# Optimization experiments

Measured on AMD Instinct MI355X. Metric: run time of the kernel, lower is better.

The kernel has to match this reference:

```python
import jax, jax.numpy as jnp
import numpy as np

B, N, C, K, D, H = 4, 16384, 256, 16, 4, 512
EPS = 1e-5


def setup_inputs() -> dict:
    key = jax.random.key(0)
    ks = jax.random.split(key, 16)
    s = 0.05  # weight scale
    inp = {
        "x": jax.random.normal(ks[0], (B, N, C), jnp.float32),
        "knn": jax.random.randint(ks[1], (B, N, K), 0, N, jnp.int32),
        "lfp_w": jax.random.normal(ks[2], (D, C, C), jnp.float32) * s,
        "lfp_bn_w": jax.random.uniform(ks[3], (D, C), jnp.float32),
        "lfp_bn_b": jax.random.normal(ks[4], (D, C), jnp.float32) * s,
        "mlp0_w1": jax.random.normal(ks[5], (C, H), jnp.float32) * s,
        "mlp0_b1": jax.random.normal(ks[6], (H,), jnp.float32) * s,
        "mlp0_w2": jax.random.normal(ks[7], (H, C), jnp.float32) * s,
        "mlp0_bn_w": jax.random.uniform(ks[8], (C,), jnp.float32),
        "mlp0_bn_b": jax.random.normal(ks[9], (C,), jnp.float32) * s,
        "mlps_w1": jax.random.normal(ks[10], (D // 2, C, H), jnp.float32) * s,
        "mlps_b1": jax.random.normal(ks[11], (D // 2, H), jnp.float32) * s,
        "mlps_w2": jax.random.normal(ks[12], (D // 2, H, C), jnp.float32) * s,
        "mlps_bn_w": jax.random.uniform(ks[13], (D // 2, C), jnp.float32),
        "mlps_bn_b": jax.random.normal(ks[14], (D // 2, C), jnp.float32) * s,
    }
    return inp


def _bn(y, w, b):
    # BatchNorm1d over flattened (B*N) rows, biased variance, train-mode stats
    m = y.mean(axis=(0, 1))
    v = ((y - m) ** 2).mean(axis=(0, 1))
    return (y - m) * jax.lax.rsqrt(v + EPS) * w + b


def _mlp(y, w1, b1, w2, bw, bb):
    h = jax.nn.gelu(jnp.einsum("bnc,ch->bnh", y, w1) + b1, approximate=False)
    return _bn(jnp.einsum("bnh,hc->bnc", h, w2), bw, bb)


def _lfp(y, knn, w, bw, bb):
    p = jnp.einsum("bnc,cd->bnd", y, w)               # linear proj, no bias
    nb = jax.vmap(lambda pb, kb: pb[kb])(p, knn)      # [B,N,K,C] neighbor gather
    return _bn(nb.max(axis=2) - p, bw, bb)            # max over knn minus self


def reference(x, knn, lfp_w, lfp_bn_w, lfp_bn_b,
              mlp0_w1, mlp0_b1, mlp0_w2, mlp0_bn_w, mlp0_bn_b,
              mlps_w1, mlps_b1, mlps_w2, mlps_bn_w, mlps_bn_b):
    # Block.forward (eval: drop_path = identity)
    x = x + _mlp(x, mlp0_w1, mlp0_b1, mlp0_w2, mlp0_bn_w, mlp0_bn_b)
    depth = lfp_w.shape[0]
    for i in range(depth):
        x = x + _lfp(x, knn, lfp_w[i], lfp_bn_w[i], lfp_bn_b[i])
        if i % 2 == 1:
            j = i // 2
            x = x + _mlp(x, mlps_w1[j], mlps_b1[j], mlps_w2[j],
                         mlps_bn_w[j], mlps_bn_b[j])
    return x
```

## Files before the change

### kernel.cpp

```cpp
#include <hip/hip_runtime.h>
#include <hip/hip_bf16.h>

#define M_TOTAL 65536
#define NPTS    16384
#define CDIM    256
#define KNN     16
#define HDIM    512
#define CSTR    136

typedef __bf16 bf16x8 __attribute__((ext_vector_type(8)));
typedef float  f32x4  __attribute__((ext_vector_type(4)));

__device__ inline float b2f(unsigned u) {
    union { unsigned v; float f; } x; x.v = u << 16; return x.f;
}
__device__ inline unsigned short f2b(float f) {
    union { float f; unsigned u; } x; x.f = f;
    unsigned r = x.u + 0x7fffu + ((x.u >> 16) & 1u);
    return (unsigned short)(r >> 16);
}
__device__ inline void gload_lds16(const void* g, void* l) {
    __builtin_amdgcn_global_load_lds(
        (const __attribute__((address_space(1))) unsigned*)g,
        (__attribute__((address_space(3))) unsigned*)l, 16, 0, 0);
}
__device__ inline float gelu_tanh(float u) {
    const float t = u * (0.7978845608f + 0.0356774081f * u * u);
    const float e = __expf(2.f * t);
    const float th = 1.f - 2.f * __builtin_amdgcn_rcpf(e + 1.f);
    return 0.5f * u * (1.f + th);
}
__device__ inline void fmax8(uint4 v, float* mx) {
    mx[0] = fmaxf(mx[0], b2f(v.x & 0xffffu)); mx[1] = fmaxf(mx[1], b2f(v.x >> 16));
    mx[2] = fmaxf(mx[2], b2f(v.y & 0xffffu)); mx[3] = fmaxf(mx[3], b2f(v.y >> 16));
    mx[4] = fmaxf(mx[4], b2f(v.z & 0xffffu)); mx[5] = fmaxf(mx[5], b2f(v.z >> 16));
    mx[6] = fmaxf(mx[6], b2f(v.w & 0xffffu)); mx[7] = fmaxf(mx[7], b2f(v.w >> 16));
}

template<int MODE>
__global__ __launch_bounds__(256) void gemm_nt(
    const short* __restrict__ A, const short* __restrict__ BT,
    short* __restrict__ outB,
    const float* __restrict__ bias, float2* __restrict__ partials,
    int N, int K)
{
    __shared__ short a_lds[128 * 32];
    __shared__ short b_lds[128 * 32];
    __shared__ short c_lds[128 * CSTR];
    __shared__ float s_sum[128], s_sq[128];

    const int tid = threadIdx.x;
    const int nx = gridDim.x, nwg = nx * gridDim.y;
    const int bid = blockIdx.y * nx + blockIdx.x;
    const int lid = (bid & 7) * (nwg >> 3) + (bid >> 3);
    const int m0 = (lid / nx) * 128, n0 = (lid % nx) * 128;

    const int w = tid >> 6, l = tid & 63;
    const int wm = w >> 1, wn = w & 1;

    if (MODE == 2 && tid < 128) { s_sum[tid] = 0.f; s_sq[tid] = 0.f; }

    f32x4 acc[4][4] = {};

    const int lrow = l & 15, lk = (l >> 4) * 8;
    const int q0 = 2 * w, q1 = 2 * w + 1;
    const int gr = l >> 2, gc = (l & 3) * 8;
    const size_t arow0 = (size_t)(m0 + q0 * 16 + gr) * K + gc;
    const size_t arow1 = (size_t)(m0 + q1 * 16 + gr) * K + gc;
    const size_t brow0 = (size_t)(n0 + q0 * 16 + gr) * K + gc;
    const size_t brow1 = (size_t)(n0 + q1 * 16 + gr) * K + gc;

    const int nkt = K >> 5;
    for (int kt = 0; kt < nkt; ++kt) {
        const int k0 = kt << 5;
        if (kt) __syncthreads();
        gload_lds16(A  + arow0 + k0, a_lds + q0 * 512);
        gload_lds16(A  + arow1 + k0, a_lds + q1 * 512);
        gload_lds16(BT + brow0 + k0, b_lds + q0 * 512);
        gload_lds16(BT + brow1 + k0, b_lds + q1 * 512);
        __syncthreads();

        bf16x8 af[4], bfr[4];
#pragma unroll
        for (int i = 0; i < 4; ++i)
            af[i] = *(const bf16x8*)(a_lds + (wm * 64 + i * 16 + lrow) * 32 + lk);
#pragma unroll
        for (int j = 0; j < 4; ++j)
            bfr[j] = *(const bf16x8*)(b_lds + (wn * 64 + j * 16 + lrow) * 32 + lk);
#pragma unroll
        for (int i = 0; i < 4; ++i)
#pragma unroll
            for (int j = 0; j < 4; ++j)
                acc[i][j] = __builtin_amdgcn_mfma_f32_16x16x32_bf16(
                    af[i], bfr[j], acc[i][j], 0, 0, 0);
    }

    const int lq = l >> 4;
#pragma unroll
    for (int j = 0; j < 4; ++j) {
        const int cl  = wn * 64 + j * 16 + lrow;
        const float bsv = (MODE == 1) ? bias[n0 + cl] : 0.f;
        float psum = 0.f, psq = 0.f;
#pragma unroll
        for (int i = 0; i < 4; ++i) {
#pragma unroll
            for (int r = 0; r < 4; ++r) {
                const int row = wm * 64 + i * 16 + lq * 4 + r;
                float v = acc[i][j][r];
                if (MODE == 1) v = gelu_tanh(v + bsv);
                c_lds[row * CSTR + cl] = (short)f2b(v);
                if (MODE == 2) { psum += v; psq += v * v; }
            }
        }
        if (MODE == 2) {
            atomicAdd(&s_sum[cl], psum);
            atomicAdd(&s_sq[cl], psq);
        }
    }
    __syncthreads();
#pragma unroll
    for (int it = 0; it < 8; ++it) {
        const int idx = it * 256 + tid;
        const int row = idx >> 4, ch = idx & 15;
        const uint4 vv = *(const uint4*)&c_lds[row * CSTR + ch * 8];
        *(uint4*)&outB[(size_t)(m0 + row) * N + n0 + ch * 8] = vv;
    }
    if (MODE == 2 && tid < 128)
        partials[(size_t)(m0 >> 7) * N + n0 + tid] =
            make_float2(s_sum[tid], s_sq[tid]);
}

__global__ __launch_bounds__(256) void gather_max(
    const short* __restrict__ p, const int* __restrict__ knn,
    short* __restrict__ yout, float2* __restrict__ partials)
{
    __shared__ float s_sum[256], s_sq[256];
    const int tid = threadIdx.x, w = tid >> 6, l = tid & 63;
    s_sum[tid] = 0.f; s_sq[tid] = 0.f;
    __syncthreads();

    const int xcd = blockIdx.x & 7, hi = blockIdx.x >> 3;
    const int gblk = (xcd >> 1) * 512 + (hi << 1) + (xcd & 1);

    const int sub = l >> 5;
    const int cl8 = (l & 31) * 8;

    float sa[8] = {}, qa[8] = {};
    for (int it = 0; it < 4; ++it) {
        const size_t g = (size_t)gblk * 32 + w * 8 + it * 2 + sub;
        const int b = (int)(g >> 14);
        const int4* kp4 = (const int4*)(knn) + g * 4;
        const int4 k0 = kp4[0], k1 = kp4[1], k2 = kp4[2], k3 = kp4[3];
        int idxs[16];
        idxs[0]=k0.x; idxs[1]=k0.y; idxs[2]=k0.z; idxs[3]=k0.w;
        idxs[4]=k1.x; idxs[5]=k1.y; idxs[6]=k1.z; idxs[7]=k1.w;
        idxs[8]=k2.x; idxs[9]=k2.y; idxs[10]=k2.z; idxs[11]=k2.w;
        idxs[12]=k3.x; idxs[13]=k3.y; idxs[14]=k3.z; idxs[15]=k3.w;
        const short* pb = p + (size_t)b * NPTS * CDIM + cl8;
        uint4 v[16];
#pragma unroll
        for (int k = 0; k < 16; ++k)
            v[k] = *(const uint4*)(pb + (size_t)idxs[k] * CDIM);
        const uint4 sv = *(const uint4*)(p + g * CDIM + cl8);

        float mx[8] = {-1e30f,-1e30f,-1e30f,-1e30f,-1e30f,-1e30f,-1e30f,-1e30f};
#pragma unroll
        for (int k = 0; k < 16; ++k) fmax8(v[k], mx);

        float t[8];
        t[0] = mx[0] - b2f(sv.x & 0xffffu); t[1] = mx[1] - b2f(sv.x >> 16);
        t[2] = mx[2] - b2f(sv.y & 0xffffu); t[3] = mx[3] - b2f(sv.y >> 16);
        t[4] = mx[4] - b2f(sv.z & 0xffffu); t[5] = mx[5] - b2f(sv.z >> 16);
        t[6] = mx[6] - b2f(sv.w & 0xffffu); t[7] = mx[7] - b2f(sv.w >> 16);

        uint4 pk;
        pk.x = (unsigned)f2b(t[0]) | ((unsigned)f2b(t[1]) << 16);
        pk.y = (unsigned)f2b(t[2]) | ((unsigned)f2b(t[3]) << 16);
        pk.z = (unsigned)f2b(t[4]) | ((unsigned)f2b(t[5]) << 16);
        pk.w = (unsigned)f2b(t[6]) | ((unsigned)f2b(t[7]) << 16);
        *(uint4*)(yout + g * CDIM + cl8) = pk;
#pragma unroll
        for (int j = 0; j < 8; ++j) { sa[j] += t[j]; qa[j] += t[j] * t[j]; }
    }
#pragma unroll
    for (int j = 0; j < 8; ++j) {
        atomicAdd(&s_sum[cl8 + j], sa[j]);
        atomicAdd(&s_sq[cl8 + j], qa[j]);
    }
    __syncthreads();
    partials[(size_t)gblk * CDIM + tid] = make_float2(s_sum[tid], s_sq[tid]);
}

__global__ __launch_bounds__(256) void reduce_stats1(
    const float2* __restrict__ partials, int nblk, float2* __restrict__ part2)
{
    const int tid = threadIdx.x;
    float s = 0.f, q = 0.f;
    for (int rb = blockIdx.x; rb < nblk; rb += 16) {
        const float2 v = partials[(size_t)rb * CDIM + tid];
        s += v.x; q += v.y;
    }
    part2[(size_t)blockIdx.x * CDIM + tid] = make_float2(s, q);
}
__global__ __launch_bounds__(256) void reduce_stats2(
    const float2* __restrict__ part2,
    const float* __restrict__ bnw, const float* __restrict__ bnb,
    float2* __restrict__ scsh)
{
    const int c = threadIdx.x;
    float s = 0.f, q = 0.f;
#pragma unroll
    for (int b = 0; b < 16; ++b) {
        const float2 v = part2[(size_t)b * CDIM + c];
        s += v.x; q += v.y;
    }
    const float invM = 1.f / 65536.f;
    const float mean = s * invM;
    const float var  = q * invM - mean * mean;
    const float istd = rsqrtf(var + 1e-5f);
    const float sc   = bnw[c] * istd;
    scsh[c] = make_float2(sc, bnb[c] - mean * sc);
}

template<int V>
__global__ __launch_bounds__(256) void bn_residual(
    const short* __restrict__ y, const short* __restrict__ xb_in,
    const float* __restrict__ xf_in, const float2* __restrict__ scsh,
    short* __restrict__ xb_out, float* __restrict__ xf_out)
{
    const size_t t = (size_t)blockIdx.x * 256 + threadIdx.x;
    const uint4 yv = ((const uint4*)y)[t];
    float xr[8];
    if (V == 1) {
        const float4 a = ((const float4*)xf_in)[2 * t];
        const float4 b = ((const float4*)xf_in)[2 * t + 1];
        xr[0]=a.x; xr[1]=a.y; xr[2]=a.z; xr[3]=a.w;
        xr[4]=b.x; xr[5]=b.y; xr[6]=b.z; xr[7]=b.w;
    } else {
        const uint4 xv = ((const uint4*)xb_in)[t];
        xr[0]=b2f(xv.x & 0xffffu); xr[1]=b2f(xv.x >> 16);
        xr[2]=b2f(xv.y & 0xffffu); xr[3]=b2f(xv.y >> 16);
        xr[4]=b2f(xv.z & 0xffffu); xr[5]=b2f(xv.z >> 16);
        xr[6]=b2f(xv.w & 0xffffu); xr[7]=b2f(xv.w >> 16);
    }
    float yr[8];
    yr[0]=b2f(yv.x & 0xffffu); yr[1]=b2f(yv.x >> 16);
    yr[2]=b2f(yv.y & 0xffffu); yr[3]=b2f(yv.y >> 16);
    yr[4]=b2f(yv.z & 0xffffu); yr[5]=b2f(yv.z >> 16);
    yr[6]=b2f(yv.w & 0xffffu); yr[7]=b2f(yv.w >> 16);

    const int c0 = (int)((t * 8) & (CDIM - 1));
    float o[8];
#pragma unroll
    for (int j = 0; j < 8; ++j) {
        const float2 sc = scsh[c0 + j];
        o[j] = xr[j] + yr[j] * sc.x + sc.y;
    }
    if (V == 2) {
        ((float4*)xf_out)[2 * t]     = make_float4(o[0], o[1], o[2], o[3]);
        ((float4*)xf_out)[2 * t + 1] = make_float4(o[4], o[5], o[6], o[7]);
    } else {
        uint4 pk;
        pk.x = (unsigned)f2b(o[0]) | ((unsigned)f2b(o[1]) << 16);
        pk.y = (unsigned)f2b(o[2]) | ((unsigned)f2b(o[3]) << 16);
        pk.z = (unsigned)f2b(o[4]) | ((unsigned)f2b(o[5]) << 16);
        pk.w = (unsigned)f2b(o[6]) | ((unsigned)f2b(o[7]) << 16);
        ((uint4*)xb_out)[t] = pk;
    }
}

__global__ __launch_bounds__(256) void cast_x(
    const float* __restrict__ x, short* __restrict__ xb)
{
    const size_t t = (size_t)blockIdx.x * 256 + threadIdx.x;
    const float4 v = ((const float4*)x)[t];
    uint2 pk;
    pk.x = (unsigned)f2b(v.x) | ((unsigned)f2b(v.y) << 16);
    pk.y = (unsigned)f2b(v.z) | ((unsigned)f2b(v.w) << 16);
    ((uint2*)xb)[t] = pk;
}

__global__ __launch_bounds__(256) void transpose_cast(
    const float* __restrict__ src, short* __restrict__ dst, int R, int Cc)
{
    const size_t base = (size_t)blockIdx.y * R * Cc;
    const int i = blockIdx.x * 256 + threadIdx.x;
    if (i < R * Cc) {
        const int r = i / Cc, c = i % Cc;
        dst[base + (size_t)c * R + r] = (short)f2b(src[base + i]);
    }
}


extern "C" void kernel_launch(void* const* d_in, const int* in_sizes, int n_in,
                              void* d_out, int out_size, void* d_ws, size_t ws_size,
                              hipStream_t stream)
{
    (void)in_sizes; (void)n_in; (void)out_size; (void)ws_size;

    const float* x_in      = (const float*)d_in[0];
    const int*   knn       = (const int*)  d_in[1];
    const float* lfp_w     = (const float*)d_in[2];
    const float* lfp_bn_w  = (const float*)d_in[3];
    const float* lfp_bn_b  = (const float*)d_in[4];
    const float* mlp0_w1   = (const float*)d_in[5];
    const float* mlp0_b1   = (const float*)d_in[6];
    const float* mlp0_w2   = (const float*)d_in[7];
    const float* mlp0_bn_w = (const float*)d_in[8];
    const float* mlp0_bn_b = (const float*)d_in[9];
    const float* mlps_w1   = (const float*)d_in[10];
    const float* mlps_b1   = (const float*)d_in[11];
    const float* mlps_w2   = (const float*)d_in[12];
    const float* mlps_bn_w = (const float*)d_in[13];
    const float* mlps_bn_b = (const float*)d_in[14];

    char* ws = (char*)d_ws;
    short*  xb       = (short*) (ws + 0);
    short*  ybB      = (short*) (ws + 33554432ull);
    short*  hp       = (short*) (ws + 67108864ull);
    float2* partials = (float2*)(ws + 134217728ull);
    float2* part2    = (float2*)(ws + 138412032ull);
    float2* scsh     = (float2*)(ws + 138444800ull);
    short*  lfpWT    = (short*) (ws + 138446848ull);
    short*  w1T0     = (short*) (ws + 138971136ull);
    short*  w2T0     = (short*) (ws + 139233280ull);
    short*  w1Ts     = (short*) (ws + 139495424ull);
    short*  w2Ts     = (short*) (ws + 140019712ull);
    float*  xout     = (float*)d_out;

    const dim3 blk(256);

    transpose_cast<<<dim3(256, 4), blk, 0, stream>>>(lfp_w,   lfpWT, 256, 256);
    transpose_cast<<<dim3(512, 1), blk, 0, stream>>>(mlp0_w1, w1T0,  256, 512);
    transpose_cast<<<dim3(512, 1), blk, 0, stream>>>(mlp0_w2, w2T0,  512, 256);
    transpose_cast<<<dim3(512, 2), blk, 0, stream>>>(mlps_w1, w1Ts,  256, 512);
    transpose_cast<<<dim3(512, 2), blk, 0, stream>>>(mlps_w2, w2Ts,  512, 256);
    cast_x<<<16384, blk, 0, stream>>>(x_in, xb);

    auto run_stats = [&](int nblk, const float* bnw, const float* bnb) {
        reduce_stats1<<<16, blk, 0, stream>>>(partials, nblk, part2);
        reduce_stats2<<<1, blk, 0, stream>>>(part2, bnw, bnb, scsh);
    };

    auto run_mlp = [&](const short* w1T, const float* b1, const short* w2T,
                       const float* bnw, const float* bnb, int variant) {
        gemm_nt<1><<<dim3(4, 512), blk, 0, stream>>>(xb, w1T, hp,  b1, nullptr, 512, 256);
        gemm_nt<2><<<dim3(2, 512), blk, 0, stream>>>(hp, w2T, ybB, nullptr, partials, 256, 512);
        run_stats(512, bnw, bnb);
        if (variant == 1)
            bn_residual<1><<<8192, blk, 0, stream>>>(ybB, nullptr, x_in, scsh, xb, nullptr);
        else if (variant == 2)
            bn_residual<2><<<8192, blk, 0, stream>>>(ybB, xb, nullptr, scsh, nullptr, xout);
        else
            bn_residual<0><<<8192, blk, 0, stream>>>(ybB, xb, nullptr, scsh, xb, nullptr);
    };

    run_mlp(w1T0, mlp0_b1, w2T0, mlp0_bn_w, mlp0_bn_b, 1);

    for (int i = 0; i < 4; ++i) {
        gemm_nt<0><<<dim3(2, 512), blk, 0, stream>>>(xb, lfpWT + (size_t)i * 65536,
                                                     hp, nullptr, nullptr, 256, 256);
        gather_max<<<2048, blk, 0, stream>>>(hp, knn, ybB, partials);
        run_stats(2048, lfp_bn_w + i * 256, lfp_bn_b + i * 256);
        bn_residual<0><<<8192, blk, 0, stream>>>(ybB, xb, nullptr, scsh, xb, nullptr);
        if (i & 1) {
            const int j = i >> 1;
            run_mlp(w1Ts + (size_t)j * 131072, mlps_b1 + j * 512,
                    w2Ts + (size_t)j * 131072,
                    mlps_bn_w + j * 256, mlps_bn_b + j * 256,
                    (i == 3) ? 2 : 0);
        }
    }
}
```

Before: 932.1 us.

## Split gather-max into two channel-half passes with nontemporal stores

The neighbor gather-max kernel now runs twice per layer, each pass covering 128 of the 256 channels. Each wavefront row reads 256 bytes instead of 512, which shrinks the working set of gathered rows per pass and may improve L2/MALL hit rates on the random knn gathers. Output and partial-stat writes use nontemporal stores so they do not evict gathered data. The cost is reading the knn indices twice and an extra kernel launch.

```diff
diff --git a/kernel.cpp b/kernel.cpp
--- a/kernel.cpp
+++ b/kernel.cpp
@@ -10,6 +10,8 @@
 
 typedef __bf16 bf16x8 __attribute__((ext_vector_type(8)));
 typedef float  f32x4  __attribute__((ext_vector_type(4)));
+typedef unsigned uintx4 __attribute__((ext_vector_type(4)));
+typedef float  floatx2 __attribute__((ext_vector_type(2)));
 
 __device__ inline float b2f(unsigned u) {
     union { unsigned v; float f; } x; x.v = u << 16; return x.f;
@@ -132,22 +134,23 @@
 
 __global__ __launch_bounds__(256) void gather_max(
     const short* __restrict__ p, const int* __restrict__ knn,
-    short* __restrict__ yout, float2* __restrict__ partials)
-{
-    __shared__ float s_sum[256], s_sq[256];
+    short* __restrict__ yout, float2* __restrict__ partials, int pass)
+{
+    __shared__ float s_sum[128], s_sq[128];
     const int tid = threadIdx.x, w = tid >> 6, l = tid & 63;
-    s_sum[tid] = 0.f; s_sq[tid] = 0.f;
+    if (tid < 128) { s_sum[tid] = 0.f; s_sq[tid] = 0.f; }
     __syncthreads();
 
     const int xcd = blockIdx.x & 7, hi = blockIdx.x >> 3;
     const int gblk = (xcd >> 1) * 512 + (hi << 1) + (xcd & 1);
 
-    const int sub = l >> 5;
-    const int cl8 = (l & 31) * 8;
+    const int r   = l >> 4;
+    const int c8  = (l & 15) * 8;
+    const int coff = pass * 128 + c8;
 
     float sa[8] = {}, qa[8] = {};
-    for (int it = 0; it < 4; ++it) {
-        const size_t g = (size_t)gblk * 32 + w * 8 + it * 2 + sub;
+    for (int it = 0; it < 2; ++it) {
+        const size_t g = (size_t)gblk * 32 + it * 16 + w * 4 + r;
         const int b = (int)(g >> 14);
         const int4* kp4 = (const int4*)(knn) + g * 4;
         const int4 k0 = kp4[0], k1 = kp4[1], k2 = kp4[2], k3 = kp4[3];
@@ -156,12 +159,12 @@
         idxs[4]=k1.x; idxs[5]=k1.y; idxs[6]=k1.z; idxs[7]=k1.w;
         idxs[8]=k2.x; idxs[9]=k2.y; idxs[10]=k2.z; idxs[11]=k2.w;
         idxs[12]=k3.x; idxs[13]=k3.y; idxs[14]=k3.z; idxs[15]=k3.w;
-        const short* pb = p + (size_t)b * NPTS * CDIM + cl8;
+        const short* pb = p + (size_t)b * NPTS * CDIM + coff;
         uint4 v[16];
 #pragma unroll
         for (int k = 0; k < 16; ++k)
             v[k] = *(const uint4*)(pb + (size_t)idxs[k] * CDIM);
-        const uint4 sv = *(const uint4*)(p + g * CDIM + cl8);
+        const uint4 sv = *(const uint4*)(p + g * CDIM + coff);
 
         float mx[8] = {-1e30f,-1e30f,-1e30f,-1e30f,-1e30f,-1e30f,-1e30f,-1e30f};
 #pragma unroll
@@ -173,22 +176,27 @@
         t[4] = mx[4] - b2f(sv.z & 0xffffu); t[5] = mx[5] - b2f(sv.z >> 16);
         t[6] = mx[6] - b2f(sv.w & 0xffffu); t[7] = mx[7] - b2f(sv.w >> 16);
 
-        uint4 pk;
-        pk.x = (unsigned)f2b(t[0]) | ((unsigned)f2b(t[1]) << 16);
-        pk.y = (unsigned)f2b(t[2]) | ((unsigned)f2b(t[3]) << 16);
-        pk.z = (unsigned)f2b(t[4]) | ((unsigned)f2b(t[5]) << 16);
-        pk.w = (unsigned)f2b(t[6]) | ((unsigned)f2b(t[7]) << 16);
-        *(uint4*)(yout + g * CDIM + cl8) = pk;
+        uintx4 pk;
+        pk[0] = (unsigned)f2b(t[0]) | ((unsigned)f2b(t[1]) << 16);
+        pk[1] = (unsigned)f2b(t[2]) | ((unsigned)f2b(t[3]) << 16);
+        pk[2] = (unsigned)f2b(t[4]) | ((unsigned)f2b(t[5]) << 16);
+        pk[3] = (unsigned)f2b(t[6]) | ((unsigned)f2b(t[7]) << 16);
+        __builtin_nontemporal_store(pk, (uintx4*)(yout + g * CDIM + coff));
 #pragma unroll
         for (int j = 0; j < 8; ++j) { sa[j] += t[j]; qa[j] += t[j] * t[j]; }
     }
 #pragma unroll
     for (int j = 0; j < 8; ++j) {
-        atomicAdd(&s_sum[cl8 + j], sa[j]);
-        atomicAdd(&s_sq[cl8 + j], qa[j]);
+        atomicAdd(&s_sum[c8 + j], sa[j]);
+        atomicAdd(&s_sq[c8 + j], qa[j]);
     }
     __syncthreads();
-    partials[(size_t)gblk * CDIM + tid] = make_float2(s_sum[tid], s_sq[tid]);
+    if (tid < 128) {
+        floatx2 pr;
+        pr[0] = s_sum[tid]; pr[1] = s_sq[tid];
+        __builtin_nontemporal_store(pr,
+            (floatx2*)(partials + (size_t)gblk * CDIM + pass * 128 + tid));
+    }
 }
 
 __global__ __launch_bounds__(256) void reduce_stats1(
@@ -360,7 +368,8 @@
     for (int i = 0; i < 4; ++i) {
         gemm_nt<0><<<dim3(2, 512), blk, 0, stream>>>(xb, lfpWT + (size_t)i * 65536,
                                                      hp, nullptr, nullptr, 256, 256);
-        gather_max<<<2048, blk, 0, stream>>>(hp, knn, ybB, partials);
+        gather_max<<<2048, blk, 0, stream>>>(hp, knn, ybB, partials, 0);
+        gather_max<<<2048, blk, 0, stream>>>(hp, knn, ybB, partials, 1);
         run_stats(2048, lfp_bn_w + i * 256, lfp_bn_b + i * 256);
         bn_residual<0><<<8192, blk, 0, stream>>>(ybB, xb, nullptr, scsh, xb, nullptr);
         if (i & 1) {
```

Result: slower. 1.134 ms (+21.6%).

## Double GEMM K-tile to 64 with XOR-swizzled LDS and aliased epilogue buffer

Applied to the files above, without the earlier changes.

The bf16 MFMA GEMM now stages 64-wide K tiles instead of 32, which halves the number of barrier-separated load iterations. LDS columns are XOR-swizzled by row to avoid bank conflicts on the fragment reads. The output staging buffer now aliases the A/B tile memory behind an added barrier, which keeps LDS use about the same and so preserves occupancy. The loads are still not double-buffered, so each tile load still stalls the compute.

```diff
diff --git a/kernel.cpp b/kernel.cpp
--- a/kernel.cpp
+++ b/kernel.cpp
@@ -44,10 +44,11 @@
     const float* __restrict__ bias, float2* __restrict__ partials,
     int N, int K)
 {
-    __shared__ short a_lds[128 * 32];
-    __shared__ short b_lds[128 * 32];
-    __shared__ short c_lds[128 * CSTR];
     __shared__ float s_sum[128], s_sq[128];
+    __shared__ __align__(1024) char smem[34816];
+    short* a_lds = (short*)smem;
+    short* b_lds = (short*)(smem + 16384);
+    short* c_lds = (short*)smem;
 
     const int tid = threadIdx.x;
     const int nx = gridDim.x, nwg = nx * gridDim.y;
@@ -62,38 +63,46 @@
 
     f32x4 acc[4][4] = {};
 
-    const int lrow = l & 15, lk = (l >> 4) * 8;
-    const int q0 = 2 * w, q1 = 2 * w + 1;
-    const int gr = l >> 2, gc = (l & 3) * 8;
-    const size_t arow0 = (size_t)(m0 + q0 * 16 + gr) * K + gc;
-    const size_t arow1 = (size_t)(m0 + q1 * 16 + gr) * K + gc;
-    const size_t brow0 = (size_t)(n0 + q0 * 16 + gr) * K + gc;
-    const size_t brow1 = (size_t)(n0 + q1 * 16 + gr) * K + gc;
-
-    const int nkt = K >> 5;
+    const int lrow = l & 15;
+    const int lkb  = (l >> 4) * 16;
+    const int swz  = (lrow & 7) << 4;
+    const int gr8 = l >> 3;
+    const int gcs = 8 * ((l & 7) ^ gr8);
+
+    const int nkt = K >> 6;
     for (int kt = 0; kt < nkt; ++kt) {
-        const int k0 = kt << 5;
+        const int k0 = kt << 6;
         if (kt) __syncthreads();
-        gload_lds16(A  + arow0 + k0, a_lds + q0 * 512);
-        gload_lds16(A  + arow1 + k0, a_lds + q1 * 512);
-        gload_lds16(BT + brow0 + k0, b_lds + q0 * 512);
-        gload_lds16(BT + brow1 + k0, b_lds + q1 * 512);
+#pragma unroll
+        for (int c = 0; c < 4; ++c) {
+            const int q = w * 4 + c;
+            gload_lds16(A  + (size_t)(m0 + q * 8 + gr8) * K + k0 + gcs,
+                        a_lds + q * 512 + l * 8);
+            gload_lds16(BT + (size_t)(n0 + q * 8 + gr8) * K + k0 + gcs,
+                        b_lds + q * 512 + l * 8);
+        }
         __syncthreads();
 
-        bf16x8 af[4], bfr[4];
-#pragma unroll
-        for (int i = 0; i < 4; ++i)
-            af[i] = *(const bf16x8*)(a_lds + (wm * 64 + i * 16 + lrow) * 32 + lk);
-#pragma unroll
-        for (int j = 0; j < 4; ++j)
-            bfr[j] = *(const bf16x8*)(b_lds + (wn * 64 + j * 16 + lrow) * 32 + lk);
-#pragma unroll
-        for (int i = 0; i < 4; ++i)
+#pragma unroll
+        for (int ks = 0; ks < 2; ++ks) {
+            const int cols = ((ks * 64 + lkb) ^ swz) >> 1;
+            bf16x8 af[4], bfr[4];
+#pragma unroll
+            for (int i = 0; i < 4; ++i)
+                af[i] = *(const bf16x8*)(a_lds + (wm * 64 + i * 16 + lrow) * 64 + cols);
 #pragma unroll
             for (int j = 0; j < 4; ++j)
-                acc[i][j] = __builtin_amdgcn_mfma_f32_16x16x32_bf16(
-                    af[i], bfr[j], acc[i][j], 0, 0, 0);
-    }
+                bfr[j] = *(const bf16x8*)(b_lds + (wn * 64 + j * 16 + lrow) * 64 + cols);
+#pragma unroll
+            for (int i = 0; i < 4; ++i)
+#pragma unroll
+                for (int j = 0; j < 4; ++j)
+                    acc[i][j] = __builtin_amdgcn_mfma_f32_16x16x32_bf16(
+                        af[i], bfr[j], acc[i][j], 0, 0, 0);
+        }
+    }
+
+    __syncthreads();
 
     const int lq = l >> 4;
 #pragma unroll
```

After: 913.0 us. -2.0%, faster.
